# Kernel optimization log

Measured on AMD Instinct MI355X. Metric: run time of the kernel, lower is better.

The kernel has to match this reference:

```python
import jax, jax.numpy as jnp
import numpy as np

B, T, H, S, P, NH, NL = 16, 4096, 1024, 16, 6, 8, 2
EPS = 1e-5

def _ln(x, g, b):
    m = x.mean(-1, keepdims=True)
    v = ((x - m) ** 2).mean(-1, keepdims=True)
    return (x - m) / jnp.sqrt(v + EPS) * g + b

def _mha(q, k, v, in_w, in_b, out_w, out_b, kpm):
    dh = H // NH
    wq, wk, wv = jnp.split(in_w, 3, axis=0)
    bq, bk, bv = jnp.split(in_b, 3, axis=0)
    qh = (q @ wq.T + bq).reshape(q.shape[0], q.shape[1], NH, dh)
    kh = (k @ wk.T + bk).reshape(k.shape[0], k.shape[1], NH, dh)
    vh = (v @ wv.T + bv).reshape(v.shape[0], v.shape[1], NH, dh)
    sc = jnp.einsum('bqhd,bkhd->bhqk', qh, kh) / np.float32(np.sqrt(dh))
    if kpm is not None:
        sc = jnp.where(kpm[:, None, None, :], -1e30, sc)
    a = jax.nn.softmax(sc, axis=-1)
    o = jnp.einsum('bhqk,bkhd->bqhd', a, vh).reshape(q.shape[0], q.shape[1], H)
    return o @ out_w.T + out_b

def _segment_pool(hidden, mask):
    # vectorized ragged per-segment mean over the valid prefix of each sequence
    L = mask.sum(-1)  # [B] valid lengths (assumed >= S)
    s = jnp.arange(S + 1, dtype=jnp.float32)
    bounds = jnp.floor(s[None, :] * L[:, None].astype(jnp.float32) / S).astype(jnp.int32)  # [B,S+1]
    pos = jnp.arange(T)
    valid = pos[None, :] < L[:, None]  # [B,T]
    seg_id = (pos[None, :, None] >= bounds[:, None, 1:S]).sum(-1)  # [B,T] in [0,S-1]
    oh = ((seg_id[:, :, None] == jnp.arange(S)) & valid[:, :, None]).astype(hidden.dtype)  # [B,T,S]
    seg_sum = jnp.einsum('bts,bth->bsh', oh, hidden)
    cnt = oh.sum(1)  # [B,S]
    seg_states = seg_sum / jnp.maximum(cnt, 1.0)[..., None]
    return seg_states, cnt > 0

def setup_inputs() -> dict:
    key = jax.random.key(0)
    ks = jax.random.split(key, 32)
    p = lambda k, shp: (jax.random.normal(k, shp, jnp.float32) * 0.02)
    token_states = jax.random.normal(ks[0], (B, T, H), jnp.float32)
    lengths = jax.random.randint(ks[1], (B,), T // 2, T + 1)
    attention_mask = (jnp.arange(T)[None, :] < lengths[:, None]).astype(jnp.int32)
    inp = dict(
        token_states=token_states, attention_mask=attention_mask,
        sa_in_w=p(ks[2], (3 * H, H)), sa_in_b=jnp.zeros((3 * H,)),
        sa_out_w=p(ks[3], (H, H)), sa_out_b=jnp.zeros((H,)),
        ln_g=jnp.ones((H,)), ln_b=jnp.zeros((H,)),
        sal_w1=p(ks[4], (H, H)), sal_b1=jnp.zeros((H,)),
        sal_w2=p(ks[5], (1, H)), sal_b2=jnp.zeros((1,)),
        plan_q=p(ks[6], (P, H)),
        qa_in_w=p(ks[7], (3 * H, H)), qa_in_b=jnp.zeros((3 * H,)),
        qa_out_w=p(ks[8], (H, H)), qa_out_b=jnp.zeros((H,)),
        r_in_w=p(ks[9], (NL, 3 * H, H)), r_in_b=jnp.zeros((NL, 3 * H)),
        r_out_w=p(ks[10], (NL, H, H)), r_out_b=jnp.zeros((NL, H)),
        r_ln1_g=jnp.ones((NL, H)), r_ln1_b=jnp.zeros((NL, H)),
        r_ln2_g=jnp.ones((NL, H)), r_ln2_b=jnp.zeros((NL, H)),
        r_w1=p(ks[11], (NL, 4 * H, H)), r_b1=jnp.zeros((NL, 4 * H)),
        r_w2=p(ks[12], (NL, H, 4 * H)), r_b2=jnp.zeros((NL, H)),
    )
    return inp

def reference(token_states, attention_mask, sa_in_w, sa_in_b, sa_out_w, sa_out_b,
              ln_g, ln_b, sal_w1, sal_b1, sal_w2, sal_b2, plan_q,
              qa_in_w, qa_in_b, qa_out_w, qa_out_b,
              r_in_w, r_in_b, r_out_w, r_out_b,
              r_ln1_g, r_ln1_b, r_ln2_g, r_ln2_b, r_w1, r_b1, r_w2, r_b2):
    seg, seg_mask = _segment_pool(token_states, attention_mask)
    kpm = ~seg_mask
    attn = _mha(seg, seg, seg, sa_in_w, sa_in_b, sa_out_w, sa_out_b, kpm)
    seg = _ln(seg + attn, ln_g, ln_b)
    h = jax.nn.gelu(seg @ sal_w1.T + sal_b1, approximate=False)
    logits = (h @ sal_w2.T + sal_b2)[..., 0]
    logits = jnp.where(seg_mask, logits, -10000.0)
    sal = jax.nn.softmax(logits, axis=-1)
    wseg = seg * sal[..., None]
    query = jnp.broadcast_to(plan_q[None], (token_states.shape[0], P, H))
    plan = _mha(query, wseg, wseg, qa_in_w, qa_in_b, qa_out_w, qa_out_b, kpm)
    for l in range(NL):  # norm_first TransformerEncoder layers
        y = _ln(plan, r_ln1_g[l], r_ln1_b[l])
        plan = plan + _mha(y, y, y, r_in_w[l], r_in_b[l], r_out_w[l], r_out_b[l], None)
        y = _ln(plan, r_ln2_g[l], r_ln2_b[l])
        y = jax.nn.gelu(y @ r_w1[l].T + r_b1[l], approximate=False) @ r_w2[l].T + r_b2[l]
        plan = plan + y
    entropy = -(sal * jnp.log(sal + 1e-8)).sum(-1).mean()
    nrm = jnp.maximum(jnp.linalg.norm(plan, axis=-1, keepdims=True), 1e-12)
    npn = plan / nrm
    sim = jnp.einsum('bph,bqh->bpq', npn, npn)
    off = sim * (1.0 - jnp.eye(P, dtype=sim.dtype))
    redundancy = (off ** 2).sum() / (plan.shape[0] * P * (P - 1))
    return plan, sal, entropy, redundancy
```

## Files before the change

### kernel.cpp

```cpp
#include <hip/hip_runtime.h>
#include <hip/hip_bf16.h>
#include <math.h>

#define BB 16
#define TT 4096
#define HH 1024
#define SS 16
#define PP 6
#define NHH 8
#define DHH 128
#define NLL 2

typedef __hip_bfloat16 bf16;

__device__ __forceinline__ float b2f(bf16 x){ return __bfloat162float(x); }
__device__ __forceinline__ float us2f(unsigned short u){ return __uint_as_float(((unsigned)u) << 16); }

template<int ISBF>
__device__ __forceinline__ float ldw(const void* p, size_t i){
    if (ISBF) return b2f(((const bf16*)p)[i]);
    else      return ((const float*)p)[i];
}

__global__ void k_init(const unsigned* __restrict__ lng, float* __restrict__ scal,
                       int* __restrict__ flag){
    if (threadIdx.x == 0){
        scal[0] = 0.f; scal[1] = 0.f; scal[2] = 0.f; scal[3] = 0.f;
        flag[0] = (lng[0] == 0x3F800000u) ? 0 : 1;
    }
}

__global__ void k_len(const int* __restrict__ mask, int* __restrict__ L){
    int b = blockIdx.x, tid = threadIdx.x;
    int s = 0;
    for (int t = tid; t < TT; t += 256) s += mask[b*TT + t];
    __shared__ int red[256];
    red[tid] = s; __syncthreads();
    for (int w = 128; w > 0; w >>= 1){ if (tid < w) red[tid] += red[tid+w]; __syncthreads(); }
    if (tid == 0) L[b] = red[0];
}

template<int ISBF>
__device__ void segpool_body(const void* __restrict__ tok, const int* __restrict__ L,
                             float* __restrict__ seg){
    int s = blockIdx.x, b = blockIdx.y;
    int len = L[b];
    int lo = (s*len)/SS, hi = ((s+1)*len)/SS;
    int tid = threadIdx.x;
    int h0 = tid*4;
    float a0=0.f,a1=0.f,a2=0.f,a3=0.f;
    if (ISBF){
        const bf16* t = (const bf16*)tok;
        for (int tt = lo; tt < hi; ++tt){
            ushort4 u = *(const ushort4*)(t + ((size_t)(b*TT + tt))*HH + h0);
            a0 += us2f(u.x); a1 += us2f(u.y); a2 += us2f(u.z); a3 += us2f(u.w);
        }
    } else {
        const float* t = (const float*)tok;
        for (int tt = lo; tt < hi; ++tt){
            float4 u = *(const float4*)(t + ((size_t)(b*TT + tt))*HH + h0);
            a0 += u.x; a1 += u.y; a2 += u.z; a3 += u.w;
        }
    }
    float inv = 1.0f/(float)(hi-lo);
    float* o = seg + ((size_t)(b*SS + s))*HH + h0;
    o[0]=a0*inv; o[1]=a1*inv; o[2]=a2*inv; o[3]=a3*inv;
}
__global__ void k_segpool(const void* __restrict__ tok, const int* __restrict__ L,
                          float* __restrict__ seg, const int* __restrict__ flag){
    if (*flag) segpool_body<1>(tok, L, seg); else segpool_body<0>(tok, L, seg);
}

__global__ __launch_bounds__(256) void k_gemmsk(
        const float* __restrict__ X, const void* __restrict__ W,
        float* __restrict__ part, int N, int K, int M,
        size_t offW, int kChunk, const int* __restrict__ flag){
    __shared__ float As[16][68], Bs[16][68];
    const int tid = threadIdx.x;
    const int r0 = blockIdx.y*64, c0 = blockIdx.x*64;
    const int tx = tid & 15, ty = tid >> 4;
    const int sr = tid >> 2;
    const int sk = (tid & 3) << 2;
    const int kbeg = blockIdx.z * kChunk, kend = kbeg + kChunk;
    const int isbf = *flag;
    float c[4][4] = {{0.f,0.f,0.f,0.f},{0.f,0.f,0.f,0.f},{0.f,0.f,0.f,0.f},{0.f,0.f,0.f,0.f}};
    for (int k0 = kbeg; k0 < kend; k0 += 16){
        float4 av = make_float4(0.f,0.f,0.f,0.f);
        if (r0 + sr < N) av = *(const float4*)(X + (size_t)(r0+sr)*K + k0 + sk);
        float4 bv;
        if (isbf){
            ushort4 u = *(const ushort4*)((const bf16*)W + offW + (size_t)(c0+sr)*K + k0 + sk);
            bv = make_float4(us2f(u.x), us2f(u.y), us2f(u.z), us2f(u.w));
        } else {
            bv = *(const float4*)((const float*)W + offW + (size_t)(c0+sr)*K + k0 + sk);
        }
        As[sk+0][sr]=av.x; As[sk+1][sr]=av.y; As[sk+2][sr]=av.z; As[sk+3][sr]=av.w;
        Bs[sk+0][sr]=bv.x; Bs[sk+1][sr]=bv.y; Bs[sk+2][sr]=bv.z; Bs[sk+3][sr]=bv.w;
        __syncthreads();
        #pragma unroll
        for (int kk = 0; kk < 16; ++kk){
            float4 a = *(const float4*)&As[kk][ty<<2];
            float4 b = *(const float4*)&Bs[kk][tx<<2];
            c[0][0] += a.x*b.x; c[0][1] += a.x*b.y; c[0][2] += a.x*b.z; c[0][3] += a.x*b.w;
            c[1][0] += a.y*b.x; c[1][1] += a.y*b.y; c[1][2] += a.y*b.z; c[1][3] += a.y*b.w;
            c[2][0] += a.z*b.x; c[2][1] += a.z*b.y; c[2][2] += a.z*b.z; c[2][3] += a.z*b.w;
            c[3][0] += a.w*b.x; c[3][1] += a.w*b.y; c[3][2] += a.w*b.z; c[3][3] += a.w*b.w;
        }
        __syncthreads();
    }
    float* dst = part + (size_t)blockIdx.z * ((size_t)N * M);
    #pragma unroll
    for (int i = 0; i < 4; ++i){
        int r = r0 + (ty<<2) + i;
        if (r < N){
            float4 st = make_float4(c[i][0], c[i][1], c[i][2], c[i][3]);
            *(float4*)(dst + (size_t)r*M + c0 + (tx<<2)) = st;
        }
    }
}

template<int ACT, int RES>
__global__ void k_epi(const float* __restrict__ part, const void* __restrict__ bias,
                      const float* __restrict__ R, float* __restrict__ Y,
                      int M, int offB, int total, int SK, const int* __restrict__ flag){
    int i = blockIdx.x*256 + threadIdx.x;
    if (i >= total) return;
    float v = 0.f;
    for (int z = 0; z < SK; ++z) v += part[(size_t)z*total + i];
    int col = i % M;
    v += (*flag) ? b2f(((const bf16*)bias)[offB + col]) : ((const float*)bias)[offB + col];
    if (ACT == 1) v = 0.5f*v*(1.0f + erff(v*0.70710678118654752f));
    if (RES == 1) v += R[i];
    Y[i] = v;
}

static void gemm_sk(hipStream_t st, const float* X, const void* W, const void* bias,
                    const float* R, float* Y, float* part, const int* flag,
                    int N, int K, int M, size_t offW, int offB, int SK, int act, int res){
    dim3 g(M/64, (N+63)/64, SK);
    k_gemmsk<<<g, 256, 0, st>>>(X, W, part, N, K, M, offW, K/SK, flag);
    int total = N*M;
    int nb = (total + 255)/256;
    if (act){
        if (res) k_epi<1,1><<<nb,256,0,st>>>(part, bias, R, Y, M, offB, total, SK, flag);
        else     k_epi<1,0><<<nb,256,0,st>>>(part, bias, R, Y, M, offB, total, SK, flag);
    } else {
        if (res) k_epi<0,1><<<nb,256,0,st>>>(part, bias, R, Y, M, offB, total, SK, flag);
        else     k_epi<0,0><<<nb,256,0,st>>>(part, bias, R, Y, M, offB, total, SK, flag);
    }
}

__global__ void k_attn(const float* __restrict__ Qb, const float* __restrict__ Kb,
                       const float* __restrict__ Vb, float* __restrict__ O,
                       int nq, int nk, int sQ, int sKV, int qShared){
    __shared__ float Qs[16][DHH], Ks[16][DHH], Vs[16][DHH];
    __shared__ float sc[16][17];
    int b = blockIdx.x / NHH, h = blockIdx.x % NHH;
    int tid = threadIdx.x;
    for (int idx = tid; idx < nq*DHH; idx += 256){
        int i = idx >> 7, d = idx & 127;
        int r = qShared ? i : (b*nq + i);
        Qs[i][d] = Qb[(size_t)r*sQ + h*DHH + d];
    }
    for (int idx = tid; idx < nk*DHH; idx += 256){
        int j = idx >> 7, d = idx & 127;
        Ks[j][d] = Kb[(size_t)(b*nk + j)*sKV + h*DHH + d];
        Vs[j][d] = Vb[(size_t)(b*nk + j)*sKV + h*DHH + d];
    }
    __syncthreads();
    const float scale = 0.0883883476483184406f;
    for (int idx = tid; idx < nq*nk; idx += 256){
        int i = idx / nk, j = idx % nk;
        float s = 0.f;
        for (int d = 0; d < DHH; ++d) s += Qs[i][d]*Ks[j][d];
        sc[i][j] = s * scale;
    }
    __syncthreads();
    if (tid < nq){
        float m = -1e30f;
        for (int j = 0; j < nk; ++j) m = fmaxf(m, sc[tid][j]);
        float ssum = 0.f;
        for (int j = 0; j < nk; ++j){ float e = expf(sc[tid][j] - m); sc[tid][j] = e; ssum += e; }
        float inv = 1.0f/ssum;
        for (int j = 0; j < nk; ++j) sc[tid][j] *= inv;
    }
    __syncthreads();
    for (int idx = tid; idx < nq*DHH; idx += 256){
        int i = idx >> 7, d = idx & 127;
        float o = 0.f;
        for (int j = 0; j < nk; ++j) o += sc[i][j]*Vs[j][d];
        O[(size_t)(b*nq + i)*HH + h*DHH + d] = o;
    }
}

template<int ISBF>
__device__ void ln_body(const float* __restrict__ X, const void* __restrict__ g,
                        const void* __restrict__ bta, float* __restrict__ Y, int off){
    int row = blockIdx.x, tid = threadIdx.x;
    const float* x = X + (size_t)row*HH;
    float v[4]; float s = 0.f, sq = 0.f;
    #pragma unroll
    for (int u = 0; u < 4; ++u){ v[u] = x[tid + u*256]; s += v[u]; sq += v[u]*v[u]; }
    __shared__ float r1[256], r2[256];
    r1[tid] = s; r2[tid] = sq; __syncthreads();
    for (int w = 128; w > 0; w >>= 1){
        if (tid < w){ r1[tid] += r1[tid+w]; r2[tid] += r2[tid+w]; }
        __syncthreads();
    }
    float mean = r1[0]*(1.0f/HH);
    float var  = fmaxf(r2[0]*(1.0f/HH) - mean*mean, 0.f);
    float rstd = rsqrtf(var + 1e-5f);
    float* y = Y + (size_t)row*HH;
    #pragma unroll
    for (int u = 0; u < 4; ++u){
        int c = tid + u*256;
        y[c] = (v[u]-mean)*rstd*ldw<ISBF>(g, (size_t)(off+c)) + ldw<ISBF>(bta, (size_t)(off+c));
    }
}
__global__ void k_ln(const float* __restrict__ X, const void* __restrict__ g,
                     const void* __restrict__ bta, float* __restrict__ Y,
                     int off, const int* __restrict__ flag){
    if (*flag) ln_body<1>(X,g,bta,Y,off); else ln_body<0>(X,g,bta,Y,off);
}

template<int ISBF>
__device__ void sal_body(const float* __restrict__ Hbuf, const void* __restrict__ w2,
                         const void* __restrict__ b2v, float* __restrict__ sal,
                         float* __restrict__ scal){
    int b = blockIdx.x, tid = threadIdx.x;
    __shared__ float red[256];
    __shared__ float lg[SS];
    for (int s = 0; s < SS; ++s){
        const float* hr = Hbuf + (size_t)(b*SS + s)*HH;
        float acc = 0.f;
        for (int k = tid; k < HH; k += 256) acc += hr[k]*ldw<ISBF>(w2, (size_t)k);
        red[tid] = acc; __syncthreads();
        for (int w = 128; w > 0; w >>= 1){ if (tid < w) red[tid] += red[tid+w]; __syncthreads(); }
        if (tid == 0) lg[s] = red[0] + ldw<ISBF>(b2v, 0);
        __syncthreads();
    }
    if (tid == 0){
        float m = -1e30f;
        for (int s = 0; s < SS; ++s) m = fmaxf(m, lg[s]);
        float ssum = 0.f;
        for (int s = 0; s < SS; ++s){ float e = expf(lg[s]-m); lg[s] = e; ssum += e; }
        float inv = 1.0f/ssum, ent = 0.f;
        for (int s = 0; s < SS; ++s){
            float p = lg[s]*inv;
            sal[b*SS+s] = p;
            ent -= p*logf(p + 1e-8f);
        }
        atomicAdd(&scal[0], ent);
    }
}
__global__ void k_sal(const float* __restrict__ Hbuf, const void* __restrict__ w2,
                      const void* __restrict__ b2v, float* __restrict__ sal,
                      float* __restrict__ scal, const int* __restrict__ flag){
    if (*flag) sal_body<1>(Hbuf,w2,b2v,sal,scal); else sal_body<0>(Hbuf,w2,b2v,sal,scal);
}

__global__ void k_wseg(const float* __restrict__ seg, const float* __restrict__ sal,
                       float* __restrict__ wseg){
    int i = blockIdx.x*256 + threadIdx.x;
    wseg[i] = seg[i]*sal[i/HH];
}

__global__ void k_cvt(const void* __restrict__ in, float* __restrict__ out, int n,
                      const int* __restrict__ flag){
    int i = blockIdx.x*256 + threadIdx.x;
    if (i < n){
        if (*flag) out[i] = b2f(((const bf16*)in)[i]);
        else       out[i] = ((const float*)in)[i];
    }
}

__global__ void k_red(const float* __restrict__ plan, float* __restrict__ scal){
    int b = blockIdx.x, tid = threadIdx.x;
    __shared__ float Pl[PP][HH];
    __shared__ float red[256];
    __shared__ float nrm[PP];
    for (int idx = tid; idx < PP*HH; idx += 256)
        Pl[idx/HH][idx%HH] = plan[(size_t)b*PP*HH + idx];
    __syncthreads();
    for (int p = 0; p < PP; ++p){
        float a = 0.f;
        for (int k = tid; k < HH; k += 256){ float v = Pl[p][k]; a += v*v; }
        red[tid] = a; __syncthreads();
        for (int w = 128; w > 0; w >>= 1){ if (tid < w) red[tid] += red[tid+w]; __syncthreads(); }
        if (tid == 0) nrm[p] = fmaxf(sqrtf(red[0]), 1e-12f);
        __syncthreads();
    }
    float total = 0.f;
    for (int p = 0; p < PP; ++p){
        for (int q = p+1; q < PP; ++q){
            float a = 0.f;
            for (int k = tid; k < HH; k += 256) a += Pl[p][k]*Pl[q][k];
            red[tid] = a; __syncthreads();
            for (int w = 128; w > 0; w >>= 1){ if (tid < w) red[tid] += red[tid+w]; __syncthreads(); }
            if (tid == 0){ float s = red[0]/(nrm[p]*nrm[q]); total += 2.0f*s*s; }
            __syncthreads();
        }
    }
    if (tid == 0) atomicAdd(&scal[1], total);
}

__global__ void k_out(const float* __restrict__ plan, const float* __restrict__ sal,
                      const float* __restrict__ scal, void* __restrict__ outv,
                      const int* __restrict__ flag){
    int i = blockIdx.x*256 + threadIdx.x;
    const int NPLAN = BB*PP*HH;
    const int NSAL  = BB*SS;
    float v;
    if (i < NPLAN) v = plan[i];
    else if (i < NPLAN + NSAL) v = sal[i - NPLAN];
    else if (i == NPLAN + NSAL) v = scal[0] * (1.0f/BB);
    else if (i == NPLAN + NSAL + 1) v = scal[1] * (1.0f/(BB*PP*(PP-1)));
    else return;
    if (*flag) ((bf16*)outv)[i] = __float2bfloat16(v);
    else       ((float*)outv)[i] = v;
}

extern "C" void kernel_launch(void* const* d_in, const int* in_sizes, int n_in,
                              void* d_out, int out_size, void* d_ws, size_t ws_size,
                              hipStream_t stream) {
    const void* tok      = d_in[0];
    const int*  mask     = (const int*)d_in[1];
    const void* sa_in_w  = d_in[2];
    const void* sa_in_b  = d_in[3];
    const void* sa_out_w = d_in[4];
    const void* sa_out_b = d_in[5];
    const void* ln_g     = d_in[6];
    const void* ln_b     = d_in[7];
    const void* sal_w1   = d_in[8];
    const void* sal_b1   = d_in[9];
    const void* sal_w2   = d_in[10];
    const void* sal_b2   = d_in[11];
    const void* plan_q   = d_in[12];
    const void* qa_in_w  = d_in[13];
    const void* qa_in_b  = d_in[14];
    const void* qa_out_w = d_in[15];
    const void* qa_out_b = d_in[16];
    const void* r_in_w   = d_in[17];
    const void* r_in_b   = d_in[18];
    const void* r_out_w  = d_in[19];
    const void* r_out_b  = d_in[20];
    const void* r_ln1_g  = d_in[21];
    const void* r_ln1_b  = d_in[22];
    const void* r_ln2_g  = d_in[23];
    const void* r_ln2_b  = d_in[24];
    const void* r_w1     = d_in[25];
    const void* r_b1     = d_in[26];
    const void* r_w2     = d_in[27];
    const void* r_b2     = d_in[28];

    float* ws   = (float*)d_ws;
    float* seg  = ws;
    float* qkv  = seg  + BB*SS*HH;
    float* t1   = qkv  + BB*SS*3*HH;
    float* t2   = t1   + BB*SS*HH;
    float* plan = t2   + BB*SS*HH;
    float* ybuf = plan + BB*PP*HH;
    float* qkv2 = ybuf + BB*PP*HH;
    float* pbuf = qkv2 + BB*PP*4*HH;
    float* sal  = pbuf + BB*PP*HH;
    float* qx   = sal  + BB*SS;
    float* qh   = qx   + PP*HH;
    float* part = qh   + PP*HH;
    float* scal = part + 2*BB*SS*3*HH;
    int*   Lw   = (int*)(scal + 4);
    int*   flag = Lw + BB;

    k_init<<<1, 64, 0, stream>>>((const unsigned*)ln_g, scal, flag);
    k_len<<<BB, 256, 0, stream>>>(mask, Lw);
    k_segpool<<<dim3(SS, BB), 256, 0, stream>>>(tok, Lw, seg, flag);

    gemm_sk(stream, seg, sa_in_w, sa_in_b, nullptr, qkv, part, flag,
            BB*SS, HH, 3*HH, (size_t)0, 0, 2, 0, 0);
    k_attn<<<BB*NHH, 256, 0, stream>>>(qkv, qkv+HH, qkv+2*HH, t1, SS, SS, 3*HH, 3*HH, 0);
    gemm_sk(stream, t1, sa_out_w, sa_out_b, seg, t2, part, flag,
            BB*SS, HH, HH, (size_t)0, 0, 4, 0, 1);
    k_ln<<<BB*SS, 256, 0, stream>>>(t2, ln_g, ln_b, seg, 0, flag);

    gemm_sk(stream, seg, sal_w1, sal_b1, nullptr, t1, part, flag,
            BB*SS, HH, HH, (size_t)0, 0, 4, 1, 0);
    k_sal<<<BB, 256, 0, stream>>>(t1, sal_w2, sal_b2, sal, scal, flag);
    k_wseg<<<BB*SS*HH/256, 256, 0, stream>>>(seg, sal, t2);

    k_cvt<<<(PP*HH+255)/256, 256, 0, stream>>>(plan_q, qx, PP*HH, flag);
    gemm_sk(stream, qx, qa_in_w, qa_in_b, nullptr, qh, part, flag,
            PP, HH, HH, (size_t)0, 0, 8, 0, 0);
    gemm_sk(stream, t2, qa_in_w, qa_in_b, nullptr, qkv, part, flag,
            BB*SS, HH, 2*HH, (size_t)HH*HH, HH, 2, 0, 0);
    k_attn<<<BB*NHH, 256, 0, stream>>>(qh, qkv, qkv+HH, pbuf, PP, SS, HH, 2*HH, 1);
    gemm_sk(stream, pbuf, qa_out_w, qa_out_b, nullptr, plan, part, flag,
            BB*PP, HH, HH, (size_t)0, 0, 8, 0, 0);

    for (int l = 0; l < NLL; ++l){
        k_ln<<<BB*PP, 256, 0, stream>>>(plan, r_ln1_g, r_ln1_b, ybuf, l*HH, flag);
        gemm_sk(stream, ybuf, r_in_w, r_in_b, nullptr, qkv2, part, flag,
                BB*PP, HH, 3*HH, (size_t)l*3*HH*HH, l*3*HH, 4, 0, 0);
        k_attn<<<BB*NHH, 256, 0, stream>>>(qkv2, qkv2+HH, qkv2+2*HH, pbuf, PP, PP, 3*HH, 3*HH, 0);
        gemm_sk(stream, pbuf, r_out_w, r_out_b, plan, plan, part, flag,
                BB*PP, HH, HH, (size_t)l*HH*HH, l*HH, 8, 0, 1);
        k_ln<<<BB*PP, 256, 0, stream>>>(plan, r_ln2_g, r_ln2_b, ybuf, l*HH, flag);
        gemm_sk(stream, ybuf, r_w1, r_b1, nullptr, qkv2, part, flag,
                BB*PP, HH, 4*HH, (size_t)l*4*HH*HH, l*4*HH, 2, 1, 0);
        gemm_sk(stream, qkv2, r_w2, r_b2, plan, plan, part, flag,
                BB*PP, 4*HH, HH, (size_t)l*HH*4*HH, l*HH, 8, 0, 1);
    }

    k_red<<<BB, 256, 0, stream>>>(plan, scal);
    k_out<<<(BB*PP*HH + BB*SS + 2 + 255)/256, 256, 0, stream>>>(plan, sal, scal, d_out, flag);
}
```

Measured before the change: 1.039 ms.

## Fuse epilogues with layernorm, parallelize segpool, reductions, and raise split-K

Fuses the split-K epilogue with the following layernorm, merges the init kernel into the length kernel, and splits segment pooling across more threads per block with a shared-memory reduction. It also vectorizes attention loads and dots with float4, splits the saliency and redundancy reductions into more parallel kernels, and raises the split-K factors along with the partial buffer size. The aim is to cut launch count and serial per-block work and to expose more parallelism for small GEMMs. In exchange there are more partial-sum reads in the epilogues and a larger workspace.

```diff
diff --git a/kernel.cpp b/kernel.cpp
--- a/kernel.cpp
+++ b/kernel.cpp
@@ -22,16 +22,14 @@
     else      return ((const float*)p)[i];
 }
 
-__global__ void k_init(const unsigned* __restrict__ lng, float* __restrict__ scal,
-                       int* __restrict__ flag){
-    if (threadIdx.x == 0){
+__global__ void k_len(const int* __restrict__ mask, int* __restrict__ L,
+                      const unsigned* __restrict__ lng, float* __restrict__ scal,
+                      int* __restrict__ flag){
+    int b = blockIdx.x, tid = threadIdx.x;
+    if (b == 0 && tid == 0){
         scal[0] = 0.f; scal[1] = 0.f; scal[2] = 0.f; scal[3] = 0.f;
         flag[0] = (lng[0] == 0x3F800000u) ? 0 : 1;
     }
-}
-
-__global__ void k_len(const int* __restrict__ mask, int* __restrict__ L){
-    int b = blockIdx.x, tid = threadIdx.x;
     int s = 0;
     for (int t = tid; t < TT; t += 256) s += mask[b*TT + t];
     __shared__ int red[256];
@@ -43,35 +41,67 @@
 template<int ISBF>
 __device__ void segpool_body(const void* __restrict__ tok, const int* __restrict__ L,
                              float* __restrict__ seg){
-    int s = blockIdx.x, b = blockIdx.y;
+    __shared__ float sm[8*1024];
+    int s = blockIdx.x, b = blockIdx.y, tid = threadIdx.x;
     int len = L[b];
     int lo = (s*len)/SS, hi = ((s+1)*len)/SS;
-    int tid = threadIdx.x;
-    int h0 = tid*4;
-    float a0=0.f,a1=0.f,a2=0.f,a3=0.f;
+    float inv = 1.0f/(float)(hi-lo);
     if (ISBF){
-        const bf16* t = (const bf16*)tok;
-        for (int tt = lo; tt < hi; ++tt){
-            ushort4 u = *(const ushort4*)(t + ((size_t)(b*TT + tt))*HH + h0);
-            a0 += us2f(u.x); a1 += us2f(u.y); a2 += us2f(u.z); a3 += us2f(u.w);
+        int ro = tid >> 7;
+        int c8 = (tid & 127) << 3;
+        float a[8];
+        #pragma unroll
+        for (int i = 0; i < 8; ++i) a[i] = 0.f;
+        const unsigned short* t = (const unsigned short*)tok;
+        for (int tt = lo + ro; tt < hi; tt += 8){
+            uint4 u = *(const uint4*)(t + ((size_t)(b*TT + tt))*HH + c8);
+            a[0] += us2f((unsigned short)(u.x & 0xffff)); a[1] += us2f((unsigned short)(u.x >> 16));
+            a[2] += us2f((unsigned short)(u.y & 0xffff)); a[3] += us2f((unsigned short)(u.y >> 16));
+            a[4] += us2f((unsigned short)(u.z & 0xffff)); a[5] += us2f((unsigned short)(u.z >> 16));
+            a[6] += us2f((unsigned short)(u.w & 0xffff)); a[7] += us2f((unsigned short)(u.w >> 16));
+        }
+        #pragma unroll
+        for (int i = 0; i < 8; ++i) sm[ro*1024 + c8 + i] = a[i];
+        __syncthreads();
+        if (ro == 0){
+            #pragma unroll
+            for (int r = 1; r < 8; ++r)
+                #pragma unroll
+                for (int i = 0; i < 8; ++i) a[i] += sm[r*1024 + c8 + i];
+            float* o = seg + ((size_t)(b*SS + s))*HH + c8;
+            #pragma unroll
+            for (int i = 0; i < 8; ++i) o[i] = a[i]*inv;
         }
     } else {
+        int ro = tid >> 8;
+        int c4 = (tid & 255) << 2;
+        float a[4] = {0.f,0.f,0.f,0.f};
         const float* t = (const float*)tok;
-        for (int tt = lo; tt < hi; ++tt){
-            float4 u = *(const float4*)(t + ((size_t)(b*TT + tt))*HH + h0);
-            a0 += u.x; a1 += u.y; a2 += u.z; a3 += u.w;
-        }
-    }
-    float inv = 1.0f/(float)(hi-lo);
-    float* o = seg + ((size_t)(b*SS + s))*HH + h0;
-    o[0]=a0*inv; o[1]=a1*inv; o[2]=a2*inv; o[3]=a3*inv;
-}
-__global__ void k_segpool(const void* __restrict__ tok, const int* __restrict__ L,
+        for (int tt = lo + ro; tt < hi; tt += 4){
+            float4 u = *(const float4*)(t + ((size_t)(b*TT + tt))*HH + c4);
+            a[0] += u.x; a[1] += u.y; a[2] += u.z; a[3] += u.w;
+        }
+        #pragma unroll
+        for (int i = 0; i < 4; ++i) sm[ro*1024 + c4 + i] = a[i];
+        __syncthreads();
+        if (ro == 0){
+            #pragma unroll
+            for (int r = 1; r < 4; ++r)
+                #pragma unroll
+                for (int i = 0; i < 4; ++i) a[i] += sm[r*1024 + c4 + i];
+            float* o = seg + ((size_t)(b*SS + s))*HH + c4;
+            #pragma unroll
+            for (int i = 0; i < 4; ++i) o[i] = a[i]*inv;
+        }
+    }
+}
+__global__ __launch_bounds__(1024) void k_segpool(const void* __restrict__ tok,
+                          const int* __restrict__ L,
                           float* __restrict__ seg, const int* __restrict__ flag){
     if (*flag) segpool_body<1>(tok, L, seg); else segpool_body<0>(tok, L, seg);
 }
 
-__global__ __launch_bounds__(256) void k_gemmsk(
+__global__ __launch_bounds__(256,2) void k_gemmsk(
         const float* __restrict__ X, const void* __restrict__ W,
         float* __restrict__ part, int N, int K, int M,
         size_t offW, int kChunk, const int* __restrict__ flag){
@@ -134,6 +164,51 @@
     Y[i] = v;
 }
 
+template<int ISBF, int RES>
+__device__ void epiln_body(const float* __restrict__ part, const void* __restrict__ bias,
+                           const float* __restrict__ R, float* __restrict__ Y,
+                           float* __restrict__ Z, const void* __restrict__ g,
+                           const void* __restrict__ bta,
+                           int offB, int lnoff, int N, int SK){
+    int row = blockIdx.x, tid = threadIdx.x;
+    size_t base = (size_t)row*HH;
+    size_t total = (size_t)N*HH;
+    float v[4]; float s = 0.f, sq = 0.f;
+    #pragma unroll
+    for (int u = 0; u < 4; ++u){
+        int c = tid + u*256;
+        float a = 0.f;
+        for (int z = 0; z < SK; ++z) a += part[(size_t)z*total + base + c];
+        a += ldw<ISBF>(bias, (size_t)(offB + c));
+        if (RES) a += R[base + c];
+        Y[base + c] = a;
+        v[u] = a; s += a; sq += a*a;
+    }
+    __shared__ float r1[256], r2[256];
+    r1[tid] = s; r2[tid] = sq; __syncthreads();
+    for (int w = 128; w > 0; w >>= 1){
+        if (tid < w){ r1[tid] += r1[tid+w]; r2[tid] += r2[tid+w]; }
+        __syncthreads();
+    }
+    float mean = r1[0]*(1.0f/HH);
+    float var  = fmaxf(r2[0]*(1.0f/HH) - mean*mean, 0.f);
+    float rstd = rsqrtf(var + 1e-5f);
+    #pragma unroll
+    for (int u = 0; u < 4; ++u){
+        int c = tid + u*256;
+        Z[base + c] = (v[u]-mean)*rstd*ldw<ISBF>(g, (size_t)(lnoff+c)) + ldw<ISBF>(bta, (size_t)(lnoff+c));
+    }
+}
+template<int RES>
+__global__ void k_epiln(const float* __restrict__ part, const void* __restrict__ bias,
+                        const float* __restrict__ R, float* __restrict__ Y,
+                        float* __restrict__ Z, const void* __restrict__ g,
+                        const void* __restrict__ bta, int offB, int lnoff, int N, int SK,
+                        const int* __restrict__ flag){
+    if (*flag) epiln_body<1,RES>(part,bias,R,Y,Z,g,bta,offB,lnoff,N,SK);
+    else       epiln_body<0,RES>(part,bias,R,Y,Z,g,bta,offB,lnoff,N,SK);
+}
+
 static void gemm_sk(hipStream_t st, const float* X, const void* W, const void* bias,
                     const float* R, float* Y, float* part, const int* flag,
                     int N, int K, int M, size_t offW, int offB, int SK, int act, int res){
@@ -150,30 +225,46 @@
     }
 }
 
+static void gemm_skln(hipStream_t st, const float* X, const void* W, const void* bias,
+                      const float* R, float* Y, float* Z, const void* g, const void* bta,
+                      float* part, const int* flag,
+                      int N, int K, int M, size_t offW, int offB, int lnoff, int SK, int res){
+    dim3 gr(M/64, (N+63)/64, SK);
+    k_gemmsk<<<gr, 256, 0, st>>>(X, W, part, N, K, M, offW, K/SK, flag);
+    if (res) k_epiln<1><<<N,256,0,st>>>(part, bias, R, Y, Z, g, bta, offB, lnoff, N, SK, flag);
+    else     k_epiln<0><<<N,256,0,st>>>(part, bias, R, Y, Z, g, bta, offB, lnoff, N, SK, flag);
+}
+
 __global__ void k_attn(const float* __restrict__ Qb, const float* __restrict__ Kb,
                        const float* __restrict__ Vb, float* __restrict__ O,
                        int nq, int nk, int sQ, int sKV, int qShared){
-    __shared__ float Qs[16][DHH], Ks[16][DHH], Vs[16][DHH];
+    __shared__ float Qs[16][132], Ks[16][132], Vs[16][132];
     __shared__ float sc[16][17];
     int b = blockIdx.x / NHH, h = blockIdx.x % NHH;
     int tid = threadIdx.x;
-    for (int idx = tid; idx < nq*DHH; idx += 256){
-        int i = idx >> 7, d = idx & 127;
+    for (int idx = tid; idx < nq*32; idx += 256){
+        int i = idx >> 5, d4 = (idx & 31) << 2;
         int r = qShared ? i : (b*nq + i);
-        Qs[i][d] = Qb[(size_t)r*sQ + h*DHH + d];
-    }
-    for (int idx = tid; idx < nk*DHH; idx += 256){
-        int j = idx >> 7, d = idx & 127;
-        Ks[j][d] = Kb[(size_t)(b*nk + j)*sKV + h*DHH + d];
-        Vs[j][d] = Vb[(size_t)(b*nk + j)*sKV + h*DHH + d];
+        *(float4*)&Qs[i][d4] = *(const float4*)&Qb[(size_t)r*sQ + h*DHH + d4];
+    }
+    for (int idx = tid; idx < nk*32; idx += 256){
+        int j = idx >> 5, d4 = (idx & 31) << 2;
+        *(float4*)&Ks[j][d4] = *(const float4*)&Kb[(size_t)(b*nk + j)*sKV + h*DHH + d4];
+        *(float4*)&Vs[j][d4] = *(const float4*)&Vb[(size_t)(b*nk + j)*sKV + h*DHH + d4];
     }
     __syncthreads();
     const float scale = 0.0883883476483184406f;
     for (int idx = tid; idx < nq*nk; idx += 256){
-        int i = idx / nk, j = idx % nk;
-        float s = 0.f;
-        for (int d = 0; d < DHH; ++d) s += Qs[i][d]*Ks[j][d];
-        sc[i][j] = s * scale;
+        int i = idx / nk, j = idx - i*nk;
+        const float4* qp = (const float4*)&Qs[i][0];
+        const float4* kp = (const float4*)&Ks[j][0];
+        float ax=0.f, ay=0.f, az=0.f, aw=0.f;
+        #pragma unroll
+        for (int k4 = 0; k4 < 32; ++k4){
+            float4 a = qp[k4], c = kp[k4];
+            ax += a.x*c.x; ay += a.y*c.y; az += a.z*c.z; aw += a.w*c.w;
+        }
+        sc[i][j] = (ax+ay+az+aw) * scale;
     }
     __syncthreads();
     if (tid < nq){
@@ -185,78 +276,54 @@
         for (int j = 0; j < nk; ++j) sc[tid][j] *= inv;
     }
     __syncthreads();
-    for (int idx = tid; idx < nq*DHH; idx += 256){
-        int i = idx >> 7, d = idx & 127;
-        float o = 0.f;
-        for (int j = 0; j < nk; ++j) o += sc[i][j]*Vs[j][d];
-        O[(size_t)(b*nq + i)*HH + h*DHH + d] = o;
+    for (int idx = tid; idx < nq*32; idx += 256){
+        int i = idx >> 5, d4 = (idx & 31) << 2;
+        float ox=0.f, oy=0.f, oz=0.f, ow=0.f;
+        for (int j = 0; j < nk; ++j){
+            float s = sc[i][j];
+            float4 v = *(const float4*)&Vs[j][d4];
+            ox += s*v.x; oy += s*v.y; oz += s*v.z; ow += s*v.w;
+        }
+        float4 o = make_float4(ox,oy,oz,ow);
+        *(float4*)&O[(size_t)(b*nq + i)*HH + h*DHH + d4] = o;
     }
 }
 
 template<int ISBF>
-__device__ void ln_body(const float* __restrict__ X, const void* __restrict__ g,
-                        const void* __restrict__ bta, float* __restrict__ Y, int off){
-    int row = blockIdx.x, tid = threadIdx.x;
-    const float* x = X + (size_t)row*HH;
-    float v[4]; float s = 0.f, sq = 0.f;
+__device__ void sallogit_body(const float* __restrict__ Hbuf, const void* __restrict__ w2,
+                              const void* __restrict__ b2v, float* __restrict__ lg){
+    int s = blockIdx.x, b = blockIdx.y, tid = threadIdx.x;
+    const float* hr = Hbuf + (size_t)(b*SS + s)*HH;
+    float acc = 0.f;
     #pragma unroll
-    for (int u = 0; u < 4; ++u){ v[u] = x[tid + u*256]; s += v[u]; sq += v[u]*v[u]; }
-    __shared__ float r1[256], r2[256];
-    r1[tid] = s; r2[tid] = sq; __syncthreads();
-    for (int w = 128; w > 0; w >>= 1){
-        if (tid < w){ r1[tid] += r1[tid+w]; r2[tid] += r2[tid+w]; }
-        __syncthreads();
-    }
-    float mean = r1[0]*(1.0f/HH);
-    float var  = fmaxf(r2[0]*(1.0f/HH) - mean*mean, 0.f);
-    float rstd = rsqrtf(var + 1e-5f);
-    float* y = Y + (size_t)row*HH;
-    #pragma unroll
-    for (int u = 0; u < 4; ++u){
-        int c = tid + u*256;
-        y[c] = (v[u]-mean)*rstd*ldw<ISBF>(g, (size_t)(off+c)) + ldw<ISBF>(bta, (size_t)(off+c));
-    }
-}
-__global__ void k_ln(const float* __restrict__ X, const void* __restrict__ g,
-                     const void* __restrict__ bta, float* __restrict__ Y,
-                     int off, const int* __restrict__ flag){
-    if (*flag) ln_body<1>(X,g,bta,Y,off); else ln_body<0>(X,g,bta,Y,off);
-}
-
-template<int ISBF>
-__device__ void sal_body(const float* __restrict__ Hbuf, const void* __restrict__ w2,
-                         const void* __restrict__ b2v, float* __restrict__ sal,
-                         float* __restrict__ scal){
-    int b = blockIdx.x, tid = threadIdx.x;
+    for (int u = 0; u < 4; ++u){ int c = tid + u*256; acc += hr[c]*ldw<ISBF>(w2, (size_t)c); }
     __shared__ float red[256];
-    __shared__ float lg[SS];
-    for (int s = 0; s < SS; ++s){
-        const float* hr = Hbuf + (size_t)(b*SS + s)*HH;
-        float acc = 0.f;
-        for (int k = tid; k < HH; k += 256) acc += hr[k]*ldw<ISBF>(w2, (size_t)k);
-        red[tid] = acc; __syncthreads();
-        for (int w = 128; w > 0; w >>= 1){ if (tid < w) red[tid] += red[tid+w]; __syncthreads(); }
-        if (tid == 0) lg[s] = red[0] + ldw<ISBF>(b2v, 0);
-        __syncthreads();
-    }
-    if (tid == 0){
+    red[tid] = acc; __syncthreads();
+    for (int w = 128; w > 0; w >>= 1){ if (tid < w) red[tid] += red[tid+w]; __syncthreads(); }
+    if (tid == 0) lg[b*SS + s] = red[0] + ldw<ISBF>(b2v, 0);
+}
+__global__ void k_sallogit(const float* __restrict__ Hbuf, const void* __restrict__ w2,
+                           const void* __restrict__ b2v, float* __restrict__ lg,
+                           const int* __restrict__ flag){
+    if (*flag) sallogit_body<1>(Hbuf,w2,b2v,lg); else sallogit_body<0>(Hbuf,w2,b2v,lg);
+}
+__global__ void k_salsm(const float* __restrict__ lg, float* __restrict__ sal,
+                        float* __restrict__ scal){
+    int b = blockIdx.x;
+    if (threadIdx.x == 0){
+        float e[SS];
         float m = -1e30f;
-        for (int s = 0; s < SS; ++s) m = fmaxf(m, lg[s]);
+        for (int s = 0; s < SS; ++s) m = fmaxf(m, lg[b*SS+s]);
         float ssum = 0.f;
-        for (int s = 0; s < SS; ++s){ float e = expf(lg[s]-m); lg[s] = e; ssum += e; }
+        for (int s = 0; s < SS; ++s){ e[s] = expf(lg[b*SS+s]-m); ssum += e[s]; }
         float inv = 1.0f/ssum, ent = 0.f;
         for (int s = 0; s < SS; ++s){
-            float p = lg[s]*inv;
+            float p = e[s]*inv;
             sal[b*SS+s] = p;
             ent -= p*logf(p + 1e-8f);
         }
         atomicAdd(&scal[0], ent);
     }
-}
-__global__ void k_sal(const float* __restrict__ Hbuf, const void* __restrict__ w2,
-                      const void* __restrict__ b2v, float* __restrict__ sal,
-                      float* __restrict__ scal, const int* __restrict__ flag){
-    if (*flag) sal_body<1>(Hbuf,w2,b2v,sal,scal); else sal_body<0>(Hbuf,w2,b2v,sal,scal);
 }
 
 __global__ void k_wseg(const float* __restrict__ seg, const float* __restrict__ sal,
@@ -274,34 +341,41 @@
     }
 }
 
-__global__ void k_red(const float* __restrict__ plan, float* __restrict__ scal){
-    int b = blockIdx.x, tid = threadIdx.x;
-    __shared__ float Pl[PP][HH];
+__device__ const int g_PR[21] = {0,1,2,3,4,5, 0,0,0,0,0,1,1,1,1,2,2,2,3,3,4};
+__device__ const int g_QR[21] = {0,1,2,3,4,5, 1,2,3,4,5,2,3,4,5,3,4,5,4,5,5};
+
+__global__ void k_dots(const float* __restrict__ plan, float* __restrict__ dots){
+    int t = blockIdx.x % 21, b = blockIdx.x / 21, tid = threadIdx.x;
+    const float* X = plan + (size_t)b*PP*HH + (size_t)g_PR[t]*HH;
+    const float* Yv = plan + (size_t)b*PP*HH + (size_t)g_QR[t]*HH;
+    float acc = 0.f;
+    #pragma unroll
+    for (int u = 0; u < 4; ++u){ int c = tid + u*256; acc += X[c]*Yv[c]; }
     __shared__ float red[256];
-    __shared__ float nrm[PP];
-    for (int idx = tid; idx < PP*HH; idx += 256)
-        Pl[idx/HH][idx%HH] = plan[(size_t)b*PP*HH + idx];
+    red[tid] = acc; __syncthreads();
+    for (int w = 128; w > 0; w >>= 1){ if (tid < w) red[tid] += red[tid+w]; __syncthreads(); }
+    if (tid == 0) dots[b*24 + t] = red[0];
+}
+__global__ void k_red2(const float* __restrict__ dots, float* __restrict__ scal){
+    __shared__ float tot[BB];
+    int tid = threadIdx.x;
+    if (tid < BB){
+        float n[PP];
+        #pragma unroll
+        for (int p = 0; p < PP; ++p) n[p] = fmaxf(sqrtf(dots[tid*24 + p]), 1e-12f);
+        float total = 0.f;
+        for (int k = 6; k < 21; ++k){
+            float s = dots[tid*24 + k] / (n[g_PR[k]]*n[g_QR[k]]);
+            total += 2.0f*s*s;
+        }
+        tot[tid] = total;
+    }
     __syncthreads();
-    for (int p = 0; p < PP; ++p){
-        float a = 0.f;
-        for (int k = tid; k < HH; k += 256){ float v = Pl[p][k]; a += v*v; }
-        red[tid] = a; __syncthreads();
-        for (int w = 128; w > 0; w >>= 1){ if (tid < w) red[tid] += red[tid+w]; __syncthreads(); }
-        if (tid == 0) nrm[p] = fmaxf(sqrtf(red[0]), 1e-12f);
-        __syncthreads();
-    }
-    float total = 0.f;
-    for (int p = 0; p < PP; ++p){
-        for (int q = p+1; q < PP; ++q){
-            float a = 0.f;
-            for (int k = tid; k < HH; k += 256) a += Pl[p][k]*Pl[q][k];
-            red[tid] = a; __syncthreads();
-            for (int w = 128; w > 0; w >>= 1){ if (tid < w) red[tid] += red[tid+w]; __syncthreads(); }
-            if (tid == 0){ float s = red[0]/(nrm[p]*nrm[q]); total += 2.0f*s*s; }
-            __syncthreads();
-        }
-    }
-    if (tid == 0) atomicAdd(&scal[1], total);
+    if (tid == 0){
+        float s = 0.f;
+        for (int i = 0; i < BB; ++i) s += tot[i];
+        scal[1] = s;
+    }
 }
 
 __global__ void k_out(const float* __restrict__ plan, const float* __restrict__ sal,
@@ -365,50 +439,55 @@
     float* sal  = pbuf + BB*PP*HH;
     float* qx   = sal  + BB*SS;
     float* qh   = qx   + PP*HH;
-    float* part = qh   + PP*HH;
-    float* scal = part + 2*BB*SS*3*HH;
+    float* lgbuf= qh   + PP*HH;
+    float* dots = lgbuf+ BB*SS;
+    float* part = dots + BB*24;
+    float* scal = part + 4*BB*SS*3*HH;
     int*   Lw   = (int*)(scal + 4);
     int*   flag = Lw + BB;
 
-    k_init<<<1, 64, 0, stream>>>((const unsigned*)ln_g, scal, flag);
-    k_len<<<BB, 256, 0, stream>>>(mask, Lw);
-    k_segpool<<<dim3(SS, BB), 256, 0, stream>>>(tok, Lw, seg, flag);
+    k_len<<<BB, 256, 0, stream>>>(mask, Lw, (const unsigned*)ln_g, scal, flag);
+    k_segpool<<<dim3(SS, BB), 1024, 0, stream>>>(tok, Lw, seg, flag);
 
     gemm_sk(stream, seg, sa_in_w, sa_in_b, nullptr, qkv, part, flag,
-            BB*SS, HH, 3*HH, (size_t)0, 0, 2, 0, 0);
+            BB*SS, HH, 3*HH, (size_t)0, 0, 4, 0, 0);
     k_attn<<<BB*NHH, 256, 0, stream>>>(qkv, qkv+HH, qkv+2*HH, t1, SS, SS, 3*HH, 3*HH, 0);
-    gemm_sk(stream, t1, sa_out_w, sa_out_b, seg, t2, part, flag,
-            BB*SS, HH, HH, (size_t)0, 0, 4, 0, 1);
-    k_ln<<<BB*SS, 256, 0, stream>>>(t2, ln_g, ln_b, seg, 0, flag);
+    gemm_skln(stream, t1, sa_out_w, sa_out_b, seg, t2, seg, ln_g, ln_b, part, flag,
+              BB*SS, HH, HH, (size_t)0, 0, 0, 8, 1);
 
     gemm_sk(stream, seg, sal_w1, sal_b1, nullptr, t1, part, flag,
-            BB*SS, HH, HH, (size_t)0, 0, 4, 1, 0);
-    k_sal<<<BB, 256, 0, stream>>>(t1, sal_w2, sal_b2, sal, scal, flag);
+            BB*SS, HH, HH, (size_t)0, 0, 8, 1, 0);
+    k_sallogit<<<dim3(SS, BB), 256, 0, stream>>>(t1, sal_w2, sal_b2, lgbuf, flag);
+    k_salsm<<<BB, 64, 0, stream>>>(lgbuf, sal, scal);
     k_wseg<<<BB*SS*HH/256, 256, 0, stream>>>(seg, sal, t2);
 
     k_cvt<<<(PP*HH+255)/256, 256, 0, stream>>>(plan_q, qx, PP*HH, flag);
     gemm_sk(stream, qx, qa_in_w, qa_in_b, nullptr, qh, part, flag,
-            PP, HH, HH, (size_t)0, 0, 8, 0, 0);
+            PP, HH, HH, (size_t)0, 0, 16, 0, 0);
     gemm_sk(stream, t2, qa_in_w, qa_in_b, nullptr, qkv, part, flag,
-            BB*SS, HH, 2*HH, (size_t)HH*HH, HH, 2, 0, 0);
+            BB*SS, HH, 2*HH, (size_t)HH*HH, HH, 4, 0, 0);
     k_attn<<<BB*NHH, 256, 0, stream>>>(qh, qkv, qkv+HH, pbuf, PP, SS, HH, 2*HH, 1);
-    gemm_sk(stream, pbuf, qa_out_w, qa_out_b, nullptr, plan, part, flag,
-            BB*PP, HH, HH, (size_t)0, 0, 8, 0, 0);
+    gemm_skln(stream, pbuf, qa_out_w, qa_out_b, nullptr, plan, ybuf, r_ln1_g, r_ln1_b,
+              part, flag, BB*PP, HH, HH, (size_t)0, 0, 0, 8, 0);
 
     for (int l = 0; l < NLL; ++l){
-        k_ln<<<BB*PP, 256, 0, stream>>>(plan, r_ln1_g, r_ln1_b, ybuf, l*HH, flag);
         gemm_sk(stream, ybuf, r_in_w, r_in_b, nullptr, qkv2, part, flag,
                 BB*PP, HH, 3*HH, (size_t)l*3*HH*HH, l*3*HH, 4, 0, 0);
         k_attn<<<BB*NHH, 256, 0, stream>>>(qkv2, qkv2+HH, qkv2+2*HH, pbuf, PP, PP, 3*HH, 3*HH, 0);
-        gemm_sk(stream, pbuf, r_out_w, r_out_b, plan, plan, part, flag,
-                BB*PP, HH, HH, (size_t)l*HH*HH, l*HH, 8, 0, 1);
-        k_ln<<<BB*PP, 256, 0, stream>>>(plan, r_ln2_g, r_ln2_b, ybuf, l*HH, flag);
+        gemm_skln(stream, pbuf, r_out_w, r_out_b, plan, plan, ybuf, r_ln2_g, r_ln2_b,
+                  part, flag, BB*PP, HH, HH, (size_t)l*HH*HH, l*HH, l*HH, 8, 1);
         gemm_sk(stream, ybuf, r_w1, r_b1, nullptr, qkv2, part, flag,
-                BB*PP, HH, 4*HH, (size_t)l*4*HH*HH, l*4*HH, 2, 1, 0);
-        gemm_sk(stream, qkv2, r_w2, r_b2, plan, plan, part, flag,
-                BB*PP, 4*HH, HH, (size_t)l*HH*4*HH, l*HH, 8, 0, 1);
-    }
-
-    k_red<<<BB, 256, 0, stream>>>(plan, scal);
+                BB*PP, HH, 4*HH, (size_t)l*4*HH*HH, l*4*HH, 4, 1, 0);
+        if (l < NLL-1){
+            gemm_skln(stream, qkv2, r_w2, r_b2, plan, plan, ybuf, r_ln1_g, r_ln1_b,
+                      part, flag, BB*PP, 4*HH, HH, (size_t)l*HH*4*HH, l*HH, (l+1)*HH, 16, 1);
+        } else {
+            gemm_sk(stream, qkv2, r_w2, r_b2, plan, plan, part, flag,
+                    BB*PP, 4*HH, HH, (size_t)l*HH*4*HH, l*HH, 16, 0, 1);
+        }
+    }
+
+    k_dots<<<BB*21, 256, 0, stream>>>(plan, dots);
+    k_red2<<<1, 64, 0, stream>>>(dots, scal);
     k_out<<<(BB*PP*HH + BB*SS + 2 + 255)/256, 256, 0, stream>>>(plan, sal, scal, d_out, flag);
 }
```

Result: faster. 882.2 us (-15.1%).
